# Optimization experiments

Measured on AMD Instinct MI355X. Metric: run time of the kernel, lower is better.

The kernel has to match this reference:

```python
import jax, jax.numpy as jnp
import numpy as np

E = 256
H = 8
DK = E // H


def setup_inputs() -> dict:
    key = jax.random.key(0)
    ks = jax.random.split(key, 16)
    B, NA, NB = 2, 2048, 2048
    x_a = jax.random.normal(ks[0], (B, NA, E), dtype=jnp.float32)
    x_b = jax.random.normal(ks[1], (B, NB, E), dtype=jnp.float32)
    s = 1.0 / np.sqrt(E)  # kaiming-normal-ish scale
    inp = {"x_a": x_a, "x_b": x_b}
    names = ["wq", "wk_a", "wk_b", "wv_a", "wv_b", "w"]
    for i, n in enumerate(names):
        inp[n + "_w"] = jax.random.normal(ks[2 + 2 * i], (E, E), dtype=jnp.float32) * s
        inp[n + "_b"] = jax.random.normal(ks[3 + 2 * i], (E,), dtype=jnp.float32) * 0.01
    return inp


def _linear(x, w, b):
    # torch nn.Linear: y = x @ w.T + b
    return jnp.einsum('bne,fe->bnf', x, w) + b


def _heads(x):
    # [B, N, E] -> [B, H, N, DK]
    B, N, _ = x.shape
    return x.reshape(B, N, H, DK).transpose(0, 2, 1, 3)


def reference(x_a, x_b, wq_w, wq_b, wk_a_w, wk_a_b, wk_b_w, wk_b_b,
              wv_a_w, wv_a_b, wv_b_w, wv_b_b, w_w, w_b):
    B, NA, _ = x_a.shape
    q = _heads(_linear(x_a, wq_w, wq_b))          # [B,H,NA,DK]
    k_a = _heads(_linear(x_a, wk_a_w, wk_a_b))    # [B,H,NA,DK]
    v_a = _heads(_linear(x_a, wv_a_w, wv_a_b))
    k_b = _heads(_linear(x_b, wk_b_w, wk_b_b))    # [B,H,NB,DK]
    v_b = _heads(_linear(x_b, wv_b_w, wv_b_b))
    k = jnp.concatenate([k_a, k_b], axis=2)       # [B,H,NA+NB,DK]
    v = jnp.concatenate([v_a, v_b], axis=2)
    scores = jnp.einsum('bhqd,bhkd->bhqk', q, k) / jnp.sqrt(jnp.float32(DK))
    p = jax.nn.softmax(scores, axis=-1)           # [B,H,NA,NA+NB]
    z = jnp.einsum('bhqk,bhkd->bhqd', p, v)       # [B,H,NA,DK]
    z = z.transpose(0, 2, 1, 3).reshape(B, NA, E)
    out = _linear(z, w_w, w_b) + x_a
    return out
```

## Files before the change

kernel.cpp:

```cpp
#include <hip/hip_runtime.h>
#include <cstdint>

typedef short bf16x8 __attribute__((ext_vector_type(8)));
typedef float f32x4 __attribute__((ext_vector_type(4)));
typedef unsigned short u16;
typedef unsigned int u32;

#define DEVI static __device__ __forceinline__


DEVI u16 f2bf(float f) {
  u32 x = __builtin_bit_cast(u32, f);
  x += 0x7fffu + ((x >> 16) & 1u);
  return (u16)(x >> 16);
}

DEVI u32 pack_bf2(float lo, float hi) {
  return (u32)f2bf(lo) | ((u32)f2bf(hi) << 16);
}

DEVI u32 cvt_pk_bf16(float lo, float hi) {
  u32 r;
  asm("v_cvt_pk_bf16_f32 %0, %1, %2" : "=v"(r) : "v"(lo), "v"(hi));
  return r;
}

DEVI f32x4 mfma16(bf16x8 a, bf16x8 b, f32x4 c) {
  return __builtin_amdgcn_mfma_f32_16x16x32_bf16(a, b, c, 0, 0, 0);
}

DEVI void load_lds16(const void* g, void* l) {
  __builtin_amdgcn_global_load_lds(
      (const __attribute__((address_space(1))) u32*)g,
      (__attribute__((address_space(3))) u32*)l, 16, 0, 0);
}

#define CSCALE 0.2550351f

__global__ __launch_bounds__(256) void convert_kernel(
    const float* __restrict__ xa, const float* __restrict__ xb,
    const float* __restrict__ w0, const float* __restrict__ w1,
    const float* __restrict__ w2, const float* __restrict__ w3,
    const float* __restrict__ w4, const float* __restrict__ w5,
    u16* __restrict__ dst) {
  int i = (int)(blockIdx.x * 256u + threadIdx.x) * 8;
  const float* s;
  if (i < 1048576) {
    s = xa + i;
  } else if (i < 2097152) {
    s = xb + (i - 1048576);
  } else {
    int t = i - 2097152;
    int j = t >> 16, o = t & 65535;
    s = (j == 0 ? w0 : j == 1 ? w1 : j == 2 ? w2 : j == 3 ? w3 : j == 4 ? w4 : w5) + o;
  }
  float4 a = *(const float4*)s;
  float4 b = *(const float4*)(s + 4);
  uint4 o4;
  o4.x = pack_bf2(a.x, a.y);
  o4.y = pack_bf2(a.z, a.w);
  o4.z = pack_bf2(b.x, b.y);
  o4.w = pack_bf2(b.z, b.w);
  *(uint4*)(dst + i) = o4;
}

__global__ __launch_bounds__(256) void proj_kernel(
    const u16* __restrict__ xa_bf, const u16* __restrict__ xb_bf,
    const u16* __restrict__ wbase,
    const float* __restrict__ b0, const float* __restrict__ b1,
    const float* __restrict__ b2, const float* __restrict__ b3,
    const float* __restrict__ b4,
    u16* __restrict__ Qo, u16* __restrict__ Ko, u16* __restrict__ Vto) {
  int job = blockIdx.z;
  const u16* A = (job <= 2) ? xa_bf : xb_bf;
  const u16* W = wbase + job * 65536;
  const float* bias = job == 0 ? b0 : job == 1 ? b1 : job == 2 ? b2 : job == 3 ? b3 : b4;
  int mode = (job == 0) ? 0 : (job == 1 || job == 3) ? 1 : 2;
  int soff = (job >= 3) ? 2048 : 0;

  int tid = threadIdx.x, wid = tid >> 6, lane = tid & 63, g = lane >> 4, c = lane & 15;
  int m0 = blockIdx.x * 64, n0 = blockIdx.y * 64;
  const u16* Ap = A + (m0 + wid * 16 + c) * 256 + g * 8;
  const u16* Wp = W + (n0 + c) * 256 + g * 8;
  f32x4 acc[4] = {};
#pragma unroll
  for (int kk = 0; kk < 256; kk += 32) {
    bf16x8 af = *(const bf16x8*)(Ap + kk);
#pragma unroll
    for (int nt = 0; nt < 4; ++nt) {
      bf16x8 bfr = *(const bf16x8*)(Wp + nt * 4096 + kk);
      acc[nt] = mfma16(af, bfr, acc[nt]);
    }
  }
#pragma unroll
  for (int nt = 0; nt < 4; ++nt) {
    int f = n0 + nt * 16 + c;
    float bv = bias[f];
    int h = f >> 5, d = f & 31;
#pragma unroll
    for (int r = 0; r < 4; ++r) {
      int m = m0 + wid * 16 + g * 4 + r;
      int bq = m >> 11, n = m & 2047;
      int bh = bq * 8 + h;
      float y = acc[nt][r] + bv;
      if (mode == 0) {
        Qo[(bh * 2048 + n) * 32 + d] = f2bf(y * CSCALE);
      } else if (mode == 1) {
        Ko[(bh * 4096 + soff + n) * 32 + d] = f2bf(y);
      } else {
        int nk = soff + n;
        int col = (nk & ~63) | ((nk & 15) << 2) | ((nk >> 4) & 3);
        Vto[(bh * 32 + d) * 4096 + col] = f2bf(y);
      }
    }
  }
}

__global__ __launch_bounds__(256) void attn_kernel(
    const u16* __restrict__ Q, const u16* __restrict__ K,
    const u16* __restrict__ Vt, u16* __restrict__ Z) {
  __shared__ __align__(16) unsigned char sbuf[25600];
  int bid = blockIdx.x;
  int xcd = bid & 7, slot = bid >> 3;
  int bh = (xcd << 1) | (slot & 1);
  int qi = slot >> 1;
  int tid = threadIdx.x, wid = tid >> 6, lane = tid & 63;
  int g = lane >> 4, c = lane & 15;
  int qbase = qi * 64 + wid * 16;

  const u16* Kbh = K + bh * (4096 * 32);
  const u16* Vtbh = Vt + bh * (32 * 4096);

  bf16x8 qf = *(const bf16x8*)(Q + (bh * 2048 + qbase + c) * 32 + g * 8);

  int kaddr = c * 64 + ((g ^ ((c >> 1) & 3)) << 4);
  int vaddr = c * 128 + ((g ^ (c & 3)) << 4) + (((c >> 2) & 1) << 6);
  unsigned char* pbuf = sbuf + 16384 + wid * 2304;
  int pwr = (g * 4) * 144 + c * 8;
  int prd = c * 144 + g * 16;

  int o = wid * 1024 + (lane << 4);
  int ko_src = o ^ (((o >> 7) & 3) << 4);
  int vd = o >> 7, vch = (o >> 4) & 7;
  int vo_src = vd * 8192 + ((vch ^ (vd & 7)) << 4);

  f32x4 z0 = {}, z1 = {};
  float lsum[4] = {0.f, 0.f, 0.f, 0.f};

  load_lds16((const unsigned char*)Kbh + ko_src, sbuf + wid * 1024);
  load_lds16((const unsigned char*)Vtbh + vo_src, sbuf + 8192 + wid * 1024);
  __syncthreads();

  for (int it = 0; it < 64; ++it) {
    int cur = it & 1;
    if (it + 1 < 64) {
      int kb = (it + 1) * 64;
      load_lds16((const unsigned char*)Kbh + kb * 64 + ko_src,
                 sbuf + (cur ^ 1) * 4096 + wid * 1024);
      load_lds16((const unsigned char*)Vtbh + kb * 2 + vo_src,
                 sbuf + 8192 + (cur ^ 1) * 4096 + wid * 1024);
    }
    const unsigned char* kbuf = sbuf + cur * 4096;
    const unsigned char* vbuf = sbuf + 8192 + cur * 4096;

    bf16x8 kf0 = *(const bf16x8*)(kbuf + kaddr);
    bf16x8 kf1 = *(const bf16x8*)(kbuf + kaddr + 1024);
    bf16x8 kf2 = *(const bf16x8*)(kbuf + kaddr + 2048);
    bf16x8 kf3 = *(const bf16x8*)(kbuf + kaddr + 3072);
    f32x4 zz = {};
    f32x4 s0 = mfma16(qf, kf0, zz);
    f32x4 s1 = mfma16(qf, kf1, zz);
    f32x4 s2 = mfma16(qf, kf2, zz);
    f32x4 s3 = mfma16(qf, kf3, zz);

    float p0[4], p1[4], p2[4], p3[4];
#pragma unroll
    for (int r = 0; r < 4; ++r) {
      p0[r] = __builtin_amdgcn_exp2f(s0[r]);
      p1[r] = __builtin_amdgcn_exp2f(s1[r]);
      p2[r] = __builtin_amdgcn_exp2f(s2[r]);
      p3[r] = __builtin_amdgcn_exp2f(s3[r]);
      lsum[r] += (p0[r] + p1[r]) + (p2[r] + p3[r]);
      *(u32*)(pbuf + pwr + r * 144) = cvt_pk_bf16(p0[r], p1[r]);
      *(u32*)(pbuf + pwr + r * 144 + 4) = cvt_pk_bf16(p2[r], p3[r]);
    }
    bf16x8 pf0 = *(const bf16x8*)(pbuf + prd);
    bf16x8 pf1 = *(const bf16x8*)(pbuf + prd + 64);
    bf16x8 vf00 = *(const bf16x8*)(vbuf + vaddr);
    bf16x8 vf01 = *(const bf16x8*)(vbuf + (vaddr ^ 64));
    bf16x8 vf10 = *(const bf16x8*)(vbuf + vaddr + 2048);
    bf16x8 vf11 = *(const bf16x8*)(vbuf + (vaddr ^ 64) + 2048);
    z0 = mfma16(pf0, vf00, z0);
    z0 = mfma16(pf1, vf01, z0);
    z1 = mfma16(pf0, vf10, z1);
    z1 = mfma16(pf1, vf11, z1);
    __syncthreads();
  }

#pragma unroll
  for (int r = 0; r < 4; ++r) {
    float t = lsum[r];
    t += __shfl_xor(t, 1);
    t += __shfl_xor(t, 2);
    t += __shfl_xor(t, 4);
    t += __shfl_xor(t, 8);
    float inv = 1.0f / t;
    int m = qbase + g * 4 + r;
    int rowbase = ((bh >> 3) * 2048 + m) * 256 + (bh & 7) * 32;
    Z[rowbase + c] = f2bf(z0[r] * inv);
    Z[rowbase + 16 + c] = f2bf(z1[r] * inv);
  }
}

__global__ __launch_bounds__(256) void out_kernel(
    const u16* __restrict__ A, const u16* __restrict__ W,
    const float* __restrict__ bias, const float* __restrict__ resid,
    float* __restrict__ out) {
  int tid = threadIdx.x, wid = tid >> 6, lane = tid & 63, g = lane >> 4, c = lane & 15;
  int m0 = blockIdx.x * 64, n0 = blockIdx.y * 64;
  const u16* Ap = A + (m0 + wid * 16 + c) * 256 + g * 8;
  const u16* Wp = W + (n0 + c) * 256 + g * 8;
  f32x4 acc[4] = {};
#pragma unroll
  for (int kk = 0; kk < 256; kk += 32) {
    bf16x8 af = *(const bf16x8*)(Ap + kk);
#pragma unroll
    for (int nt = 0; nt < 4; ++nt) {
      bf16x8 bfr = *(const bf16x8*)(Wp + nt * 4096 + kk);
      acc[nt] = mfma16(af, bfr, acc[nt]);
    }
  }
#pragma unroll
  for (int nt = 0; nt < 4; ++nt) {
    int f = n0 + nt * 16 + c;
    float bv = bias[f];
#pragma unroll
    for (int r = 0; r < 4; ++r) {
      int m = m0 + wid * 16 + g * 4 + r;
      out[m * 256 + f] = acc[nt][r] + bv + resid[m * 256 + f];
    }
  }
}

extern "C" void kernel_launch(void* const* d_in, const int* in_sizes, int n_in,
                              void* d_out, int out_size, void* d_ws, size_t ws_size,
                              hipStream_t stream) {
  const float* xa = (const float*)d_in[0];
  const float* xb = (const float*)d_in[1];
  const float* wq_w = (const float*)d_in[2];
  const float* wq_b = (const float*)d_in[3];
  const float* wka_w = (const float*)d_in[4];
  const float* wka_b = (const float*)d_in[5];
  const float* wkb_w = (const float*)d_in[6];
  const float* wkb_b = (const float*)d_in[7];
  const float* wva_w = (const float*)d_in[8];
  const float* wva_b = (const float*)d_in[9];
  const float* wvb_w = (const float*)d_in[10];
  const float* wvb_b = (const float*)d_in[11];
  const float* w_w = (const float*)d_in[12];
  const float* w_b = (const float*)d_in[13];

  u16* ws = (u16*)d_ws;
  u16* xa_bf = ws;
  u16* xb_bf = ws + 1048576;
  u16* wbf = ws + 2097152;
  u16* Qb = ws + 2490368;
  u16* Kb = ws + 3538944;
  u16* Vtb = ws + 5636096;
  u16* Zb = ws + 7733248;

  convert_kernel<<<1216, 256, 0, stream>>>(xa, xb, wq_w, wka_w, wva_w, wkb_w,
                                           wvb_w, w_w, ws);
  proj_kernel<<<dim3(64, 4, 5), 256, 0, stream>>>(
      xa_bf, xb_bf, wbf, wq_b, wka_b, wva_b, wkb_b, wvb_b, Qb, Kb, Vtb);
  attn_kernel<<<512, 256, 0, stream>>>(Qb, Kb, Vtb, Zb);
  out_kernel<<<dim3(64, 4), 256, 0, stream>>>(Zb, wbf + 5 * 65536, w_b, xa,
                                              (float*)d_out);
}
```

Baseline: 91.74 us.

## Split attention keys across two blocks and merge partials in output projection

Attention work is split along the key dimension into two halves, doubling the grid to 1024 blocks. Each block writes unnormalized fp32 partial outputs and row sums, and the output-projection kernel combines them and normalizes before the MFMA. The attention loop also moves to a triple-buffered LDS pipeline that uses explicit vmcnt waits and a single barrier per iteration, with setprio around the MFMAs. The aim is better occupancy and load hiding, at the cost of extra fp32 partial traffic and more work in the out kernel. The split is only valid because the softmax uses no max subtraction (the scores are pre-scaled), so the two partial sums can simply be added.

```diff
diff --git a/kernel.cpp b/kernel.cpp
--- a/kernel.cpp
+++ b/kernel.cpp
@@ -118,25 +118,28 @@
 
 __global__ __launch_bounds__(256) void attn_kernel(
     const u16* __restrict__ Q, const u16* __restrict__ K,
-    const u16* __restrict__ Vt, u16* __restrict__ Z) {
-  __shared__ __align__(16) unsigned char sbuf[25600];
+    const u16* __restrict__ Vt, float* __restrict__ Zp, float* __restrict__ S) {
+  __shared__ __align__(16) unsigned char sbuf[33792];
   int bid = blockIdx.x;
   int xcd = bid & 7, slot = bid >> 3;
   int bh = (xcd << 1) | (slot & 1);
-  int qi = slot >> 1;
+  int rem = slot >> 1;
+  int ks = rem & 1, qi = rem >> 1;
   int tid = threadIdx.x, wid = tid >> 6, lane = tid & 63;
   int g = lane >> 4, c = lane & 15;
   int qbase = qi * 64 + wid * 16;
 
-  const u16* Kbh = K + bh * (4096 * 32);
-  const u16* Vtbh = Vt + bh * (32 * 4096);
-
-  bf16x8 qf = *(const bf16x8*)(Q + (bh * 2048 + qbase + c) * 32 + g * 8);
+  const unsigned char* Kb =
+      (const unsigned char*)K + ((size_t)bh * 4096 + ks * 2048) * 64;
+  const unsigned char* Vb =
+      (const unsigned char*)Vt + ((size_t)bh * 32 * 4096 + ks * 2048) * 2;
+
+  bf16x8 qf = *(const bf16x8*)(Q + ((size_t)bh * 2048 + qbase + c) * 32 + g * 8);
 
   int kaddr = c * 64 + ((g ^ ((c >> 1) & 3)) << 4);
   int vaddr = c * 128 + ((g ^ (c & 3)) << 4) + (((c >> 2) & 1) << 6);
-  unsigned char* pbuf = sbuf + 16384 + wid * 2304;
-  int pwr = (g * 4) * 144 + c * 8;
+  unsigned char* pbuf = sbuf + 24576 + wid * 2304;
+  int pwr = g * 576 + c * 8;
   int prd = c * 144 + g * 16;
 
   int o = wid * 1024 + (lane << 4);
@@ -147,31 +150,40 @@
   f32x4 z0 = {}, z1 = {};
   float lsum[4] = {0.f, 0.f, 0.f, 0.f};
 
-  load_lds16((const unsigned char*)Kbh + ko_src, sbuf + wid * 1024);
-  load_lds16((const unsigned char*)Vtbh + vo_src, sbuf + 8192 + wid * 1024);
-  __syncthreads();
-
-  for (int it = 0; it < 64; ++it) {
-    int cur = it & 1;
-    if (it + 1 < 64) {
-      int kb = (it + 1) * 64;
-      load_lds16((const unsigned char*)Kbh + kb * 64 + ko_src,
-                 sbuf + (cur ^ 1) * 4096 + wid * 1024);
-      load_lds16((const unsigned char*)Vtbh + kb * 2 + vo_src,
-                 sbuf + 8192 + (cur ^ 1) * 4096 + wid * 1024);
-    }
+  load_lds16(Kb + ko_src, sbuf + wid * 1024);
+  load_lds16(Vb + vo_src, sbuf + 12288 + wid * 1024);
+
+  int cur = 0;
+  for (int t = 0; t < 32; ++t) {
+    int nxt = cur + 1;
+    if (nxt == 3) nxt = 0;
+    if (t + 1 < 32) {
+      load_lds16(Kb + (t + 1) * 4096 + ko_src, sbuf + nxt * 4096 + wid * 1024);
+      load_lds16(Vb + (t + 1) * 128 + vo_src,
+                 sbuf + 12288 + nxt * 4096 + wid * 1024);
+      __builtin_amdgcn_sched_barrier(0);
+      asm volatile("s_waitcnt vmcnt(2)" ::: "memory");
+    } else {
+      __builtin_amdgcn_sched_barrier(0);
+      asm volatile("s_waitcnt vmcnt(0)" ::: "memory");
+    }
+    __builtin_amdgcn_s_barrier();
+    __builtin_amdgcn_sched_barrier(0);
+
     const unsigned char* kbuf = sbuf + cur * 4096;
-    const unsigned char* vbuf = sbuf + 8192 + cur * 4096;
+    const unsigned char* vbuf = sbuf + 12288 + cur * 4096;
 
     bf16x8 kf0 = *(const bf16x8*)(kbuf + kaddr);
     bf16x8 kf1 = *(const bf16x8*)(kbuf + kaddr + 1024);
     bf16x8 kf2 = *(const bf16x8*)(kbuf + kaddr + 2048);
     bf16x8 kf3 = *(const bf16x8*)(kbuf + kaddr + 3072);
     f32x4 zz = {};
+    __builtin_amdgcn_s_setprio(1);
     f32x4 s0 = mfma16(qf, kf0, zz);
     f32x4 s1 = mfma16(qf, kf1, zz);
     f32x4 s2 = mfma16(qf, kf2, zz);
     f32x4 s3 = mfma16(qf, kf3, zz);
+    __builtin_amdgcn_s_setprio(0);
 
     float p0[4], p1[4], p2[4], p3[4];
 #pragma unroll
@@ -181,8 +193,10 @@
       p2[r] = __builtin_amdgcn_exp2f(s2[r]);
       p3[r] = __builtin_amdgcn_exp2f(s3[r]);
       lsum[r] += (p0[r] + p1[r]) + (p2[r] + p3[r]);
-      *(u32*)(pbuf + pwr + r * 144) = cvt_pk_bf16(p0[r], p1[r]);
-      *(u32*)(pbuf + pwr + r * 144 + 4) = cvt_pk_bf16(p2[r], p3[r]);
+      uint2 pw;
+      pw.x = cvt_pk_bf16(p0[r], p1[r]);
+      pw.y = cvt_pk_bf16(p2[r], p3[r]);
+      *(uint2*)(pbuf + pwr + r * 144) = pw;
     }
     bf16x8 pf0 = *(const bf16x8*)(pbuf + prd);
     bf16x8 pf1 = *(const bf16x8*)(pbuf + prd + 64);
@@ -190,54 +204,73 @@
     bf16x8 vf01 = *(const bf16x8*)(vbuf + (vaddr ^ 64));
     bf16x8 vf10 = *(const bf16x8*)(vbuf + vaddr + 2048);
     bf16x8 vf11 = *(const bf16x8*)(vbuf + (vaddr ^ 64) + 2048);
+    __builtin_amdgcn_s_setprio(1);
     z0 = mfma16(pf0, vf00, z0);
     z0 = mfma16(pf1, vf01, z0);
     z1 = mfma16(pf0, vf10, z1);
     z1 = mfma16(pf1, vf11, z1);
-    __syncthreads();
-  }
-
+    __builtin_amdgcn_s_setprio(0);
+    cur = nxt;
+  }
+
+  size_t zrow = ((size_t)ks * 16 + bh) * 2048;
 #pragma unroll
   for (int r = 0; r < 4; ++r) {
-    float t = lsum[r];
-    t += __shfl_xor(t, 1);
-    t += __shfl_xor(t, 2);
-    t += __shfl_xor(t, 4);
-    t += __shfl_xor(t, 8);
-    float inv = 1.0f / t;
+    float tsum = lsum[r];
+    tsum += __shfl_xor(tsum, 1);
+    tsum += __shfl_xor(tsum, 2);
+    tsum += __shfl_xor(tsum, 4);
+    tsum += __shfl_xor(tsum, 8);
     int m = qbase + g * 4 + r;
-    int rowbase = ((bh >> 3) * 2048 + m) * 256 + (bh & 7) * 32;
-    Z[rowbase + c] = f2bf(z0[r] * inv);
-    Z[rowbase + 16 + c] = f2bf(z1[r] * inv);
-  }
-}
-
-__global__ __launch_bounds__(256) void out_kernel(
-    const u16* __restrict__ A, const u16* __restrict__ W,
-    const float* __restrict__ bias, const float* __restrict__ resid,
-    float* __restrict__ out) {
+    float* zp = Zp + (zrow + m) * 32;
+    zp[c] = z0[r];
+    zp[16 + c] = z1[r];
+    if (c == 0) S[zrow + m] = tsum;
+  }
+}
+
+__global__ __launch_bounds__(512) void out_kernel(
+    const float* __restrict__ Zp, const float* __restrict__ S,
+    const u16* __restrict__ W, const float* __restrict__ bias,
+    const float* __restrict__ resid, float* __restrict__ out) {
   int tid = threadIdx.x, wid = tid >> 6, lane = tid & 63, g = lane >> 4, c = lane & 15;
   int m0 = blockIdx.x * 64, n0 = blockIdx.y * 64;
-  const u16* Ap = A + (m0 + wid * 16 + c) * 256 + g * 8;
-  const u16* Wp = W + (n0 + c) * 256 + g * 8;
-  f32x4 acc[4] = {};
-#pragma unroll
-  for (int kk = 0; kk < 256; kk += 32) {
-    bf16x8 af = *(const bf16x8*)(Ap + kk);
-#pragma unroll
-    for (int nt = 0; nt < 4; ++nt) {
-      bf16x8 bfr = *(const bf16x8*)(Wp + nt * 4096 + kk);
+  int mw = m0 + (wid & 3) * 16;
+  int nb = n0 + (wid >> 2) * 32;
+  int mrow = mw + c;
+  int bq = mrow >> 11, n = mrow & 2047;
+  const u16* Wp = W + (nb + c) * 256 + g * 8;
+  f32x4 acc[2] = {};
+#pragma unroll
+  for (int h = 0; h < 8; ++h) {
+    int bh = bq * 8 + h;
+    const float* za = Zp + ((size_t)bh * 2048 + n) * 32 + g * 8;
+    const float* zb = za + (size_t)16 * 2048 * 32;
+    float4 a0 = *(const float4*)za;
+    float4 a1 = *(const float4*)(za + 4);
+    float4 b0 = *(const float4*)zb;
+    float4 b1 = *(const float4*)(zb + 4);
+    float inv = 1.0f / (S[(size_t)bh * 2048 + n] + S[(size_t)(16 + bh) * 2048 + n]);
+    union { u32 u[4]; bf16x8 v; } cv;
+    cv.u[0] = pack_bf2((a0.x + b0.x) * inv, (a0.y + b0.y) * inv);
+    cv.u[1] = pack_bf2((a0.z + b0.z) * inv, (a0.w + b0.w) * inv);
+    cv.u[2] = pack_bf2((a1.x + b1.x) * inv, (a1.y + b1.y) * inv);
+    cv.u[3] = pack_bf2((a1.z + b1.z) * inv, (a1.w + b1.w) * inv);
+    bf16x8 af = cv.v;
+#pragma unroll
+    for (int nt = 0; nt < 2; ++nt) {
+      bf16x8 bfr = *(const bf16x8*)(Wp + nt * 4096 + h * 32);
       acc[nt] = mfma16(af, bfr, acc[nt]);
     }
   }
 #pragma unroll
-  for (int nt = 0; nt < 4; ++nt) {
-    int f = n0 + nt * 16 + c;
+  for (int nt = 0; nt < 2; ++nt) {
+    int f = nb + nt * 16 + c;
     float bv = bias[f];
 #pragma unroll
     for (int r = 0; r < 4; ++r) {
-      int m = m0 + wid * 16 + g * 4 + r;
-      out[m * 256 + f] = acc[nt][r] + bv + resid[m * 256 + f];
+      int m = mw + g * 4 + r;
+      out[(size_t)m * 256 + f] = acc[nt][r] + bv + resid[(size_t)m * 256 + f];
     }
   }
 }
@@ -267,13 +300,14 @@
   u16* Qb = ws + 2490368;
   u16* Kb = ws + 3538944;
   u16* Vtb = ws + 5636096;
-  u16* Zb = ws + 7733248;
+  float* Zp = (float*)(ws + 7733248);
+  float* S = (float*)((char*)d_ws + 23855104);
 
   convert_kernel<<<1216, 256, 0, stream>>>(xa, xb, wq_w, wka_w, wva_w, wkb_w,
                                            wvb_w, w_w, ws);
   proj_kernel<<<dim3(64, 4, 5), 256, 0, stream>>>(
       xa_bf, xb_bf, wbf, wq_b, wka_b, wva_b, wkb_b, wvb_b, Qb, Kb, Vtb);
-  attn_kernel<<<512, 256, 0, stream>>>(Qb, Kb, Vtb, Zb);
-  out_kernel<<<dim3(64, 4), 256, 0, stream>>>(Zb, wbf + 5 * 65536, w_b, xa,
+  attn_kernel<<<1024, 256, 0, stream>>>(Qb, Kb, Vtb, Zp, S);
+  out_kernel<<<dim3(64, 4), 512, 0, stream>>>(Zp, S, wbf + 5 * 65536, w_b, xa,
                                               (float*)d_out);
 }
```

Measured after the change: 86.76 us. -5.4%, faster.
